# Kernel optimization log

Measured on AMD Instinct MI355X. Metric: run time of the kernel, lower is better.

## Reference

```python
import jax, jax.numpy as jnp
import numpy as np

B, CIN, COUT, K, E, H, W = 32, 128, 256, 3, 8, 64, 64


def setup_inputs() -> dict:
    key = jax.random.key(0)
    k1, k2, k3, k4 = jax.random.split(key, 4)
    x = jax.random.normal(k1, (B, CIN, H, W), dtype=jnp.float32)
    expert_weight = jax.random.normal(k2, (E, COUT, CIN, K, K), dtype=jnp.float32)
    # nn.Linear(in_channels, num_experts): weight [E, CIN], bias [E]
    bound = 1.0 / np.sqrt(CIN)
    routing_w = jax.random.uniform(k3, (E, CIN), minval=-bound, maxval=bound, dtype=jnp.float32)
    routing_b = jax.random.uniform(k4, (E,), minval=-bound, maxval=bound, dtype=jnp.float32)
    return {"x": x, "expert_weight": expert_weight, "routing_w": routing_w, "routing_b": routing_b}


def reference(x, expert_weight, routing_w, routing_b):
    # routing: global-avg-pool -> linear -> softmax over experts
    pooled = x.mean(axis=(2, 3))                             # [B, CIN]
    logits = pooled @ routing_w.T + routing_b                # [B, E]
    rweights = jax.nn.softmax(logits, axis=-1)               # [B, E]
    # per-sample combined conv weights: [B, COUT, CIN, K, K]
    cw = jnp.einsum('be,eoikl->boikl', rweights, expert_weight)

    def conv_one(xi, wi):
        # xi: [CIN, H, W], wi: [COUT, CIN, K, K]; VALID conv, stride 1
        return jax.lax.conv_general_dilated(
            xi[None], wi, window_strides=(1, 1), padding='VALID',
            dimension_numbers=('NCHW', 'OIHW', 'NCHW'))[0]

    return jax.vmap(conv_one)(x, cw)                         # [B, COUT, H-K+1, W-K+1]
```

## Files before the change

### kernel.cpp

```cpp
#include <hip/hip_runtime.h>
#include <hip/hip_bf16.h>


#define CC_B    32
#define CC_CIN  128
#define CC_COUT 256
#define CC_NP   3844
#define CC_NT   18

typedef __attribute__((ext_vector_type(8))) short bf16x8;
typedef __attribute__((ext_vector_type(4))) float f32x4;

__global__ void cc_nhwc(const float* __restrict__ x, __hip_bfloat16* __restrict__ xn,
                        float* __restrict__ psum) {
    const int b = blockIdx.x >> 6, y = blockIdx.x & 63;
    __shared__ float lds[64 * 129];
    __shared__ float sred[256];
    const int t = threadIdx.x;
    const float* src = x + (size_t)b * CC_CIN * 4096 + y * 64;
#pragma unroll
    for (int i = 0; i < 32; ++i) {
        const int idx = i * 256 + t;
        const int cin = idx >> 6, xx = idx & 63;
        lds[xx * 129 + cin] = src[(size_t)cin * 4096 + xx];
    }
    __syncthreads();
    __hip_bfloat16* dst = xn + ((size_t)b * 4096 + y * 64) * CC_CIN;
#pragma unroll
    for (int j = 0; j < 4; ++j) {
        const int cidx = j * 256 + t;
        const int xx = cidx >> 4, c8 = (cidx & 15) * 8;
        union { __hip_bfloat16 h[8]; uint4 v; } u;
#pragma unroll
        for (int jj = 0; jj < 8; ++jj) u.h[jj] = __float2bfloat16(lds[xx * 129 + c8 + jj]);
        *reinterpret_cast<uint4*>(dst + (size_t)xx * CC_CIN + c8) = u.v;
    }
    const int cin = t & 127, xh = (t >> 7) * 32;
    float s = 0.f;
#pragma unroll
    for (int xx = 0; xx < 32; ++xx) s += lds[(xh + xx) * 129 + cin];
    sred[t] = s;
    __syncthreads();
    if (t < 128) psum[((size_t)b * 64 + y) * CC_CIN + t] = sred[t] + sred[t + 128];
}

__global__ void cc_reduce(const float* __restrict__ psum, float* __restrict__ pooled) {
    const int b = blockIdx.x, c = threadIdx.x;
    const float* p = psum + (size_t)b * 64 * CC_CIN + c;
    float s = 0.f;
#pragma unroll 8
    for (int y = 0; y < 64; ++y) s += p[(size_t)y * CC_CIN];
    pooled[b * CC_CIN + c] = s * (1.f / 4096.f);
}

__global__ void cc_routing(const float* __restrict__ pooled,
                           const float* __restrict__ rw_w,
                           const float* __restrict__ rw_b,
                           float* __restrict__ rweights) {
    const int t = threadIdx.x;
    const int b = t >> 3, e = t & 7;
    const float* p = pooled + b * CC_CIN;
    const float* w = rw_w + e * CC_CIN;
    float acc = rw_b[e];
#pragma unroll 8
    for (int i = 0; i < CC_CIN; ++i) acc += p[i] * w[i];
    float m = acc;
#pragma unroll
    for (int off = 1; off < 8; off <<= 1) m = fmaxf(m, __shfl_xor(m, off, 64));
    const float ex = __expf(acc - m);
    float sum = ex;
#pragma unroll
    for (int off = 1; off < 8; off <<= 1) sum += __shfl_xor(sum, off, 64);
    rweights[t] = ex / sum;
}

__global__ void cc_combine(const float* __restrict__ ew,
                           const float* __restrict__ rw,
                           __hip_bfloat16* __restrict__ cw) {
    const int t9 = blockIdx.x >> 8;
    const int cout = blockIdx.x & 255;
    const int cin = threadIdx.x;
    __shared__ float rws[256];
    rws[cin] = rw[cin];
    rws[cin + 128] = rw[cin + 128];
    __syncthreads();
    float wv[8];
    const size_t base = ((size_t)cout * CC_CIN + cin) * 9 + t9;
#pragma unroll
    for (int e = 0; e < 8; ++e) wv[e] = ew[base + (size_t)e * (CC_COUT * CC_CIN * 9)];
#pragma unroll 4
    for (int b = 0; b < CC_B; ++b) {
        float acc = 0.f;
#pragma unroll
        for (int e = 0; e < 8; ++e) acc += rws[b * 8 + e] * wv[e];
        cw[(((size_t)b * 9 + t9) * CC_COUT + cout) * CC_CIN + cin] = __float2bfloat16(acc);
    }
}

__device__ __forceinline__ void gload_lds16(const void* g, void* l) {
    __builtin_amdgcn_global_load_lds(
        (const __attribute__((address_space(1))) unsigned int*)g,
        (__attribute__((address_space(3))) unsigned int*)l, 16, 0, 0);
}

__global__ __launch_bounds__(256, 2) void cc_conv(
    const __hip_bfloat16* __restrict__ xn,
    const __hip_bfloat16* __restrict__ cw,
    float* __restrict__ out)
{
    __shared__ __align__(16) char smem[65536];
    const int l   = blockIdx.x;
    const int xcd = l & 7, li = l >> 3;
    const int b   = 4 * xcd + li / 62;
    const int r2  = li % 62;
    const int m0  = (r2 & 1) * 128;
    const int n0  = (r2 >> 1) * 128;

    const int tid = threadIdx.x;
    const int wid = tid >> 6, lane = tid & 63;
    const int waveM = wid >> 1, waveN = wid & 1;

    f32x4 acc[4][4];
#pragma unroll
    for (int i = 0; i < 4; ++i)
#pragma unroll
        for (int j = 0; j < 4; ++j) acc[i][j] = (f32x4){0.f, 0.f, 0.f, 0.f};

    const int gsw = (lane & 7) ^ (lane >> 3);
    int laOff[4], lbOff[4];
#pragma unroll
    for (int i = 0; i < 4; ++i) {
        const int row = wid * 32 + i * 8 + (lane >> 3);
        laOff[i] = (m0 + row) * CC_CIN + gsw * 8;
        int p = n0 + row; if (p > CC_NP - 1) p = CC_NP - 1;
        const int oy = p / 62, ox = p - oy * 62;
        lbOff[i] = (oy * 64 + ox) * CC_CIN + gsw * 8;
    }

    const __hip_bfloat16* cwb = cw + (size_t)b * 9 * CC_COUT * CC_CIN;
    const __hip_bfloat16* xnb = xn + (size_t)b * 4096 * CC_CIN;

    auto stageK = [&](int t) {
        const int t9 = t >> 1;
        const int ky = (t9 * 11) >> 5;
        const int kx = t9 - ky * 3;
        const int aoff = t9 * (CC_COUT * CC_CIN) + (t & 1) * 64;
        const int boff = (ky * 64 + kx) * CC_CIN + (t & 1) * 64;
        char* Ab = smem + (t & 1) * 16384 + wid * 4096;
        char* Bb = smem + 32768 + (t & 1) * 16384 + wid * 4096;
#pragma unroll
        for (int i = 0; i < 4; ++i)
            gload_lds16(cwb + aoff + laOff[i], Ab + i * 1024);
#pragma unroll
        for (int i = 0; i < 4; ++i)
            gload_lds16(xnb + boff + lbOff[i], Bb + i * 1024);
    };

    const int rl = lane & 15, q = lane >> 4;

    stageK(0);
    stageK(1);

#pragma unroll 1
    for (int t = 0; t < CC_NT; ++t) {
        const char* Ab = smem + (t & 1) * 16384;
        const char* Bb = smem + 32768 + (t & 1) * 16384;

        if (t < CC_NT - 1) asm volatile("s_waitcnt vmcnt(8)" ::: "memory");
        else               asm volatile("s_waitcnt vmcnt(0)" ::: "memory");
        asm volatile("s_barrier" ::: "memory");

        bf16x8 af[8], bf[8];
#pragma unroll
        for (int mf = 0; mf < 4; ++mf)
#pragma unroll
            for (int kk = 0; kk < 2; ++kk) {
                const int r = waveM * 64 + mf * 16 + rl;
                af[mf * 2 + kk] = *(const bf16x8*)(Ab + r * 128 + (((kk * 4 + q) ^ (r & 7)) * 16));
            }
#pragma unroll
        for (int nf = 0; nf < 4; ++nf)
#pragma unroll
            for (int kk = 0; kk < 2; ++kk) {
                const int r = waveN * 64 + nf * 16 + rl;
                bf[nf * 2 + kk] = *(const bf16x8*)(Bb + r * 128 + (((kk * 4 + q) ^ (r & 7)) * 16));
            }
#pragma unroll
        for (int mf = 0; mf < 4; ++mf)
#pragma unroll
            for (int nf = 0; nf < 4; ++nf)
#pragma unroll
                for (int kk = 0; kk < 2; ++kk)
                    acc[mf][nf] = __builtin_amdgcn_mfma_f32_16x16x32_bf16(
                        af[mf * 2 + kk], bf[nf * 2 + kk], acc[mf][nf], 0, 0, 0);

        asm volatile("s_waitcnt lgkmcnt(0)" ::: "memory");
        asm volatile("s_barrier" ::: "memory");
        if (t + 2 < CC_NT) stageK(t + 2);
    }

    const int q4 = (lane >> 4) * 4;
#pragma unroll
    for (int mf = 0; mf < 4; ++mf) {
        const int crow = m0 + waveM * 64 + mf * 16 + q4;
#pragma unroll
        for (int nf = 0; nf < 4; ++nf) {
            const int p = n0 + waveN * 64 + nf * 16 + (lane & 15);
            if (p < CC_NP) {
                const size_t ob = ((size_t)b * CC_COUT + crow) * CC_NP + p;
#pragma unroll
                for (int j = 0; j < 4; ++j) out[ob + (size_t)j * CC_NP] = acc[mf][nf][j];
            }
        }
    }
}

extern "C" void kernel_launch(void* const* d_in, const int* in_sizes, int n_in,
                              void* d_out, int out_size, void* d_ws, size_t ws_size,
                              hipStream_t stream) {
    const float* x   = (const float*)d_in[0];
    const float* ew  = (const float*)d_in[1];
    const float* rww = (const float*)d_in[2];
    const float* rwb = (const float*)d_in[3];
    float* out = (float*)d_out;
    char* ws = (char*)d_ws;

    __hip_bfloat16* xnhwc = (__hip_bfloat16*)ws;
    __hip_bfloat16* cwcmb = (__hip_bfloat16*)(ws + 33554432);
    float* psum   = (float*)(ws + 52428800);
    float* pooled = (float*)(ws + 53477376);
    float* rwts   = (float*)(ws + 53493760);

    cc_nhwc<<<dim3(CC_B * 64), dim3(256), 0, stream>>>(x, xnhwc, psum);
    cc_reduce<<<dim3(CC_B), dim3(128), 0, stream>>>(psum, pooled);
    cc_routing<<<dim3(1), dim3(256), 0, stream>>>(pooled, rww, rwb, rwts);
    cc_combine<<<dim3(9 * CC_COUT), dim3(128), 0, stream>>>(ew, rwts, cwcmb);
    cc_conv<<<dim3(1984), dim3(256), 0, stream>>>(xnhwc, cwcmb, out);
}
```

Measured before the change: 127.2 us.

## Keep conv input rows resident in LDS and fuse pooling reduce with routing

The conv kernel now uses 512-thread blocks, each covering 128 output channels by 4 output rows (248 pixels). It loads the 6 needed input rows once into a 96KB LDS region and reuses them across all 9 filter taps, so only the weight tiles are streamed each K-step instead of re-gathering the B operand per tap. The grid drops from 1984 to 1024 blocks at one block per CU. The pooled-mean reduction and the routing softmax are merged into one kernel, removing a launch. The change uses more LDS and lowers occupancy, and it replaces the old 128-pixel N tiles with 248-pixel tiles that pad a partial last fragment.

```diff
diff --git a/kernel.cpp b/kernel.cpp
--- a/kernel.cpp
+++ b/kernel.cpp
@@ -44,34 +44,37 @@
     if (t < 128) psum[((size_t)b * 64 + y) * CC_CIN + t] = sred[t] + sred[t + 128];
 }
 
-__global__ void cc_reduce(const float* __restrict__ psum, float* __restrict__ pooled) {
+__global__ void cc_route(const float* __restrict__ psum,
+                         const float* __restrict__ rw_w,
+                         const float* __restrict__ rw_b,
+                         float* __restrict__ rweights) {
     const int b = blockIdx.x, c = threadIdx.x;
+    __shared__ float pl[128];
+    __shared__ float lg[8];
     const float* p = psum + (size_t)b * 64 * CC_CIN + c;
     float s = 0.f;
 #pragma unroll 8
     for (int y = 0; y < 64; ++y) s += p[(size_t)y * CC_CIN];
-    pooled[b * CC_CIN + c] = s * (1.f / 4096.f);
-}
-
-__global__ void cc_routing(const float* __restrict__ pooled,
-                           const float* __restrict__ rw_w,
-                           const float* __restrict__ rw_b,
-                           float* __restrict__ rweights) {
-    const int t = threadIdx.x;
-    const int b = t >> 3, e = t & 7;
-    const float* p = pooled + b * CC_CIN;
-    const float* w = rw_w + e * CC_CIN;
-    float acc = rw_b[e];
+    pl[c] = s * (1.f / 4096.f);
+    __syncthreads();
+    if (c < 8) {
+        const float* w = rw_w + c * CC_CIN;
+        float a = rw_b[c];
 #pragma unroll 8
-    for (int i = 0; i < CC_CIN; ++i) acc += p[i] * w[i];
-    float m = acc;
-#pragma unroll
-    for (int off = 1; off < 8; off <<= 1) m = fmaxf(m, __shfl_xor(m, off, 64));
-    const float ex = __expf(acc - m);
-    float sum = ex;
-#pragma unroll
-    for (int off = 1; off < 8; off <<= 1) sum += __shfl_xor(sum, off, 64);
-    rweights[t] = ex / sum;
+        for (int i = 0; i < CC_CIN; ++i) a += pl[i] * w[i];
+        lg[c] = a;
+    }
+    __syncthreads();
+    if (c == 0) {
+        float m = lg[0];
+#pragma unroll
+        for (int e = 1; e < 8; ++e) m = fmaxf(m, lg[e]);
+        float ex[8], sm = 0.f;
+#pragma unroll
+        for (int e = 0; e < 8; ++e) { ex[e] = __expf(lg[e] - m); sm += ex[e]; }
+#pragma unroll
+        for (int e = 0; e < 8; ++e) rweights[b * 8 + e] = ex[e] / sm;
+    }
 }
 
 __global__ void cc_combine(const float* __restrict__ ew,
@@ -103,22 +106,24 @@
         (__attribute__((address_space(3))) unsigned int*)l, 16, 0, 0);
 }
 
-__global__ __launch_bounds__(256, 2) void cc_conv(
+__global__ __launch_bounds__(512, 1) void cc_conv(
     const __hip_bfloat16* __restrict__ xn,
     const __hip_bfloat16* __restrict__ cw,
     float* __restrict__ out)
 {
-    __shared__ __align__(16) char smem[65536];
+    __shared__ __align__(16) char smem[131072];
     const int l   = blockIdx.x;
     const int xcd = l & 7, li = l >> 3;
-    const int b   = 4 * xcd + li / 62;
-    const int r2  = li % 62;
-    const int m0  = (r2 & 1) * 128;
-    const int n0  = (r2 >> 1) * 128;
+    const int b   = 4 * xcd + (li >> 5);
+    const int r2  = li & 31;
+    const int nt  = r2 >> 1, mt = r2 & 1;
+    const int m0  = mt * 128;
+    const int n0  = nt * 248;
+    const int y0  = nt * 4;
 
     const int tid = threadIdx.x;
     const int wid = tid >> 6, lane = tid & 63;
-    const int waveM = wid >> 1, waveN = wid & 1;
+    const int waveM = wid >> 2, waveN = wid & 3;
 
     f32x4 acc[4][4];
 #pragma unroll
@@ -127,46 +132,58 @@
         for (int j = 0; j < 4; ++j) acc[i][j] = (f32x4){0.f, 0.f, 0.f, 0.f};
 
     const int gsw = (lane & 7) ^ (lane >> 3);
-    int laOff[4], lbOff[4];
-#pragma unroll
-    for (int i = 0; i < 4; ++i) {
-        const int row = wid * 32 + i * 8 + (lane >> 3);
-        laOff[i] = (m0 + row) * CC_CIN + gsw * 8;
-        int p = n0 + row; if (p > CC_NP - 1) p = CC_NP - 1;
-        const int oy = p / 62, ox = p - oy * 62;
-        lbOff[i] = (oy * 64 + ox) * CC_CIN + gsw * 8;
-    }
-
     const __hip_bfloat16* cwb = cw + (size_t)b * 9 * CC_COUT * CC_CIN;
     const __hip_bfloat16* xnb = xn + (size_t)b * 4096 * CC_CIN;
 
-    auto stageK = [&](int t) {
+    char* Bres = smem + 32768;
+#pragma unroll
+    for (int i = 0; i < 12; ++i) {
+        const int idx = i * 8 + wid;
+        const int h = idx / 48, rem = idx - h * 48;
+        const int yy = rem >> 3, xb = rem & 7;
+        const int x = xb * 8 + (lane >> 3);
+        int yin = y0 + yy; if (yin > 63) yin = 63;
+        gload_lds16(xnb + ((size_t)yin * 64 + x) * CC_CIN + h * 64 + gsw * 8,
+                    Bres + idx * 1024);
+    }
+
+    int laOff[2];
+#pragma unroll
+    for (int i = 0; i < 2; ++i) {
+        const int row = wid * 16 + i * 8 + (lane >> 3);
+        laOff[i] = (m0 + row) * CC_CIN + gsw * 8;
+    }
+    auto stageA = [&](int t) {
+        const int t9 = t >> 1;
+        const int aoff = t9 * (CC_COUT * CC_CIN) + (t & 1) * 64;
+        char* Ab = smem + (t & 1) * 16384 + wid * 2048;
+#pragma unroll
+        for (int i = 0; i < 2; ++i)
+            gload_lds16(cwb + aoff + laOff[i], Ab + i * 1024);
+    };
+    stageA(0);
+    stageA(1);
+
+    const int rl = lane & 15, q = lane >> 4;
+    int oyl[4], oxl[4];
+#pragma unroll
+    for (int nf = 0; nf < 4; ++nf) {
+        int c = waveN * 64 + nf * 16 + rl;
+        if (c > 247) c = 247;
+        const int oy = c / 62;
+        oyl[nf] = oy;
+        oxl[nf] = c - 62 * oy;
+    }
+
+#pragma unroll 1
+    for (int t = 0; t < CC_NT; ++t) {
+        const char* Ab = smem + (t & 1) * 16384;
         const int t9 = t >> 1;
         const int ky = (t9 * 11) >> 5;
         const int kx = t9 - ky * 3;
-        const int aoff = t9 * (CC_COUT * CC_CIN) + (t & 1) * 64;
-        const int boff = (ky * 64 + kx) * CC_CIN + (t & 1) * 64;
-        char* Ab = smem + (t & 1) * 16384 + wid * 4096;
-        char* Bb = smem + 32768 + (t & 1) * 16384 + wid * 4096;
-#pragma unroll
-        for (int i = 0; i < 4; ++i)
-            gload_lds16(cwb + aoff + laOff[i], Ab + i * 1024);
-#pragma unroll
-        for (int i = 0; i < 4; ++i)
-            gload_lds16(xnb + boff + lbOff[i], Bb + i * 1024);
-    };
-
-    const int rl = lane & 15, q = lane >> 4;
-
-    stageK(0);
-    stageK(1);
-
-#pragma unroll 1
-    for (int t = 0; t < CC_NT; ++t) {
-        const char* Ab = smem + (t & 1) * 16384;
-        const char* Bb = smem + 32768 + (t & 1) * 16384;
-
-        if (t < CC_NT - 1) asm volatile("s_waitcnt vmcnt(8)" ::: "memory");
+        const int h = t & 1;
+
+        if (t < CC_NT - 1) asm volatile("s_waitcnt vmcnt(2)" ::: "memory");
         else               asm volatile("s_waitcnt vmcnt(0)" ::: "memory");
         asm volatile("s_barrier" ::: "memory");
 
@@ -179,24 +196,25 @@
                 af[mf * 2 + kk] = *(const bf16x8*)(Ab + r * 128 + (((kk * 4 + q) ^ (r & 7)) * 16));
             }
 #pragma unroll
-        for (int nf = 0; nf < 4; ++nf)
-#pragma unroll
-            for (int kk = 0; kk < 2; ++kk) {
-                const int r = waveN * 64 + nf * 16 + rl;
-                bf[nf * 2 + kk] = *(const bf16x8*)(Bb + r * 128 + (((kk * 4 + q) ^ (r & 7)) * 16));
-            }
-#pragma unroll
-        for (int mf = 0; mf < 4; ++mf)
-#pragma unroll
-            for (int nf = 0; nf < 4; ++nf)
-#pragma unroll
-                for (int kk = 0; kk < 2; ++kk)
+        for (int nf = 0; nf < 4; ++nf) {
+            const int x = oxl[nf] + kx;
+            const int row = (h * 6 + oyl[nf] + ky) * 64 + x;
+#pragma unroll
+            for (int kk = 0; kk < 2; ++kk)
+                bf[nf * 2 + kk] = *(const bf16x8*)(Bres + row * 128 + (((kk * 4 + q) ^ (x & 7)) * 16));
+        }
+#pragma unroll
+        for (int kk = 0; kk < 2; ++kk)
+#pragma unroll
+            for (int mf = 0; mf < 4; ++mf)
+#pragma unroll
+                for (int nf = 0; nf < 4; ++nf)
                     acc[mf][nf] = __builtin_amdgcn_mfma_f32_16x16x32_bf16(
                         af[mf * 2 + kk], bf[nf * 2 + kk], acc[mf][nf], 0, 0, 0);
 
         asm volatile("s_waitcnt lgkmcnt(0)" ::: "memory");
         asm volatile("s_barrier" ::: "memory");
-        if (t + 2 < CC_NT) stageK(t + 2);
+        if (t + 2 < CC_NT) stageA(t + 2);
     }
 
     const int q4 = (lane >> 4) * 4;
@@ -205,8 +223,9 @@
         const int crow = m0 + waveM * 64 + mf * 16 + q4;
 #pragma unroll
         for (int nf = 0; nf < 4; ++nf) {
-            const int p = n0 + waveN * 64 + nf * 16 + (lane & 15);
-            if (p < CC_NP) {
+            const int c = waveN * 64 + nf * 16 + (lane & 15);
+            const int p = n0 + c;
+            if (c < 248 && p < CC_NP) {
                 const size_t ob = ((size_t)b * CC_COUT + crow) * CC_NP + p;
 #pragma unroll
                 for (int j = 0; j < 4; ++j) out[ob + (size_t)j * CC_NP] = acc[mf][nf][j];
@@ -228,12 +247,10 @@
     __hip_bfloat16* xnhwc = (__hip_bfloat16*)ws;
     __hip_bfloat16* cwcmb = (__hip_bfloat16*)(ws + 33554432);
     float* psum   = (float*)(ws + 52428800);
-    float* pooled = (float*)(ws + 53477376);
     float* rwts   = (float*)(ws + 53493760);
 
     cc_nhwc<<<dim3(CC_B * 64), dim3(256), 0, stream>>>(x, xnhwc, psum);
-    cc_reduce<<<dim3(CC_B), dim3(128), 0, stream>>>(psum, pooled);
-    cc_routing<<<dim3(1), dim3(256), 0, stream>>>(pooled, rww, rwb, rwts);
+    cc_route<<<dim3(CC_B), dim3(128), 0, stream>>>(psum, rww, rwb, rwts);
     cc_combine<<<dim3(9 * CC_COUT), dim3(128), 0, stream>>>(ew, rwts, cwcmb);
-    cc_conv<<<dim3(1984), dim3(256), 0, stream>>>(xnhwc, cwcmb, out);
-}
+    cc_conv<<<dim3(1024), dim3(512), 0, stream>>>(xnhwc, cwcmb, out);
+}
```

Result: slower. 129.8 us (+2.1%).
